# Kernel tuning notes

Hardware: AMD Instinct MI355X
Metric: run time of the kernel (lower is better)

Reference implementation:

```python
import jax, jax.numpy as jnp
import numpy as np

EULER = 0.5772156649015329  # Euler-Mascheroni constant


def _expi_neg(t):
    """Ei(t) for t < 0, via Ei(t) = -E1(-t).

    E1 uses the power series for x < 8 and the asymptotic expansion for x >= 8.
    This replaces the scipy.special.expi CPU round-trip of the original module.
    """
    x = -t  # x > 0
    # --- series branch (x < 8): E1(x) = -gamma - ln(x) + sum_{k>=1} (-1)^{k+1} x^k/(k*k!)
    xs = jnp.minimum(x, 8.0)
    s = jnp.zeros_like(xs)
    term = xs  # (-1)^{k+1} xs^k / k!  starting at k=1
    for k in range(1, 31):
        s = s + term / k
        term = term * (-xs) / (k + 1)
    e1_small = -EULER - jnp.log(xs) + s
    # --- asymptotic branch (x >= 8): E1(x) ~ e^{-x}/x * sum_n (-1)^n n! / x^n
    xl = jnp.maximum(x, 8.0)
    a = jnp.ones_like(xl)
    acc = jnp.ones_like(xl)
    for n in range(1, 9):
        a = a * (-n) / xl
        acc = acc + a
    e1_large = jnp.exp(-xl) / xl * acc
    e1 = jnp.where(x < 8.0, e1_small, e1_large)
    return -e1


def _li(v):
    # logarithmic integral li(v) = Ei(ln v); constant w.r.t. params (scipy detaches in torch)
    return jax.lax.stop_gradient(_expi_neg(jnp.log(v)))


def _phi(u, var2, var3, var4, var5):
    log_term = jnp.log(1.0 - u)
    li_term = _li(1.0 - u)
    return (var2 / log_term
            + var3 * li_term
            + var4 * ((1.0 - u) / log_term - li_term)
            + var5 * ((1.0 - u) * (log_term + 1.0) / (2.0 * log_term ** 2) - li_term / 2.0))


def setup_inputs() -> dict:
    key = jax.random.key(0)
    B, L, D = 262144, 64, 32
    hidden = [128, 128, 64]
    ks = jax.random.split(key, 16)
    u = jax.random.uniform(ks[0], (B, L), dtype=jnp.float32, minval=1e-4, maxval=1.0 - 1e-4)
    dims = [L] + hidden + [D]
    inp = {"u": u}
    for i in range(4):
        inp[f"W{i}"] = jax.random.normal(ks[1 + 2 * i], (dims[i], dims[i + 1]), dtype=jnp.float32) / np.sqrt(dims[i]).astype(np.float32)
        inp[f"b{i}"] = jnp.zeros((dims[i + 1],), dtype=jnp.float32)
    for j in range(1, 7):
        inp[f"var{j}"] = jax.random.normal(ks[8 + j], (1, D), dtype=jnp.float32) * 0.1
    return inp


def reference(u, W0, b0, W1, b1, W2, b2, W3, b3, var1, var2, var3, var4, var5, var6):
    # MLP: three Linear+ReLU blocks then final Linear to dim_data
    h = u
    for W, b in ((W0, b0), (W1, b1), (W2, b2)):
        h = jax.nn.relu(h @ W + b)
    net = h @ W3 + b3  # (B, dim_data)
    D = net.shape[1]
    ud = u[:, :D]
    # spline corrections
    p01 = -4.0 * ud ** 5 + 5.0 * ud ** 4
    corr1 = jnp.nan_to_num(p01 * (var1 + _phi(ud, var2, var3, var4, var5)), nan=0.0)
    corr2 = var6 * (ud ** 3 - 2.0 * ud ** 2 + ud)
    net_tif = jax.nn.relu(net + corr1 + corr2)
    # inverse TIF activation: ((1 - u^2)/2)^{-x}
    return jnp.power((1.0 - ud ** 2) / 2.0, -net_tif)
```

## Files before the change

kernel.cpp:

```cpp
#include <hip/hip_runtime.h>
#include <hip/hip_bf16.h>
#include <math.h>

#define FLT_MAX_F 3.4028234663852886e38f
#define PITCH_H 136

typedef _Float16 half8 __attribute__((ext_vector_type(8)));
typedef __attribute__((ext_vector_type(4))) float f32x4;
typedef __attribute__((ext_vector_type(8))) short short8;

__global__ void prep_weights(const float* __restrict__ W0, const float* __restrict__ W1,
                             const float* __restrict__ W2, const float* __restrict__ W3,
                             short* __restrict__ ws) {
    int e = blockIdx.x * 256 + threadIdx.x;
    const float* W; int N, NT, base, ul;
    if (e < 1024)      { W = W0; N = 128; NT = 8; base = 0;     ul = e; }
    else if (e < 3072) { W = W1; N = 128; NT = 8; base = 8192;  ul = e - 1024; }
    else if (e < 4096) { W = W2; N = 64;  NT = 4; base = 24576; ul = e - 3072; }
    else if (e < 4352) { W = W3; N = 32;  NT = 2; base = 32768; ul = e - 4096; }
    else return;
    const int cp = ul >> 6, lane = ul & 63;
    const int s = cp / NT, ct = cp % NT;
    const int k0 = s * 32 + (lane >> 4) * 8;
    const int n = ct * 16 + (lane & 15);
    union { half8 h; short8 s; } v;
#pragma unroll
    for (int j = 0; j < 8; ++j) v.h[j] = (_Float16)W[(size_t)(k0 + j) * N + n];
    *(short8*)(ws + base + cp * 512 + lane * 8) = v.s;
}

template <int K, int N, int G>
__device__ __forceinline__ void layer_frag(const half8* __restrict__ wf,
                                           const float* __restrict__ bias,
                                           const half8 af[K / 32], int lane, int m,
                                           f32x4* acc) {
    constexpr int NK = K / 32, NT = N / 16, CP = NK * NT, NG = CP / G;
    static_assert(CP % G == 0, "group must divide chunk count");
    half8 buf[2][G];
#pragma unroll
    for (int i = 0; i < G; ++i) buf[0][i] = wf[i * 64 + lane];
#pragma unroll
    for (int ct = 0; ct < NT; ++ct) {
        float b = bias[ct * 16 + m];
        acc[ct] = f32x4{b, b, b, b};
    }
#pragma unroll
    for (int g = 0; g < NG; ++g) {
        constexpr int dummy = 0; (void)dummy;
        const int cur = g & 1, nxt = cur ^ 1;
        if (g + 1 < NG) {
#pragma unroll
            for (int i = 0; i < G; ++i)
                buf[nxt][i] = wf[(size_t)((g + 1) * G + i) * 64 + lane];
        }
#pragma unroll
        for (int i = 0; i < G; ++i) {
            const int cp = g * G + i, s = cp / NT, ct = cp % NT;
            acc[ct] = __builtin_amdgcn_mfma_f32_16x16x32_f16(af[s], buf[cur][i], acc[ct], 0, 0, 0);
        }
    }
}

template <int K>
__device__ __forceinline__ void load_a_lds(const _Float16* __restrict__ lw, int m, int q,
                                           half8 af[K / 32]) {
    const _Float16* rp = lw + m * PITCH_H + q * 8;
#pragma unroll
    for (int s = 0; s < K / 32; ++s) af[s] = *(const half8*)(rp + s * 32);
}

template <int N>
__device__ __forceinline__ void store_d_lds(_Float16* __restrict__ lw, int m, int q,
                                            const f32x4* acc, bool relu) {
#pragma unroll
    for (int ct = 0; ct < N / 16; ++ct) {
#pragma unroll
        for (int r = 0; r < 4; ++r) {
            float v = acc[ct][r];
            if (relu) v = fmaxf(v, 0.0f);
            lw[(q * 4 + r) * PITCH_H + ct * 16 + m] = (_Float16)v;
        }
    }
}

__device__ __forceinline__ float expi_neg_fast(float t) {
    float x = -t;
    float e1s = -__logf(x) + (-0.57721566f + x * (0.99999193f + x * (-0.24991055f
              + x * (0.05519968f + x * (-0.00976004f + x * 0.00107857f)))));
    float num = 0.2677737343f + x * (8.6347608925f + x * (18.0590169730f
              + x * (8.5733287401f + x)));
    float den = 3.9584969228f + x * (21.0996530827f + x * (25.6329561486f
              + x * (9.5733223454f + x)));
    float e1l = __expf(-x) * num * __builtin_amdgcn_rcpf(x * den);
    float e1 = (x < 1.0f) ? e1s : e1l;
    return -e1;
}

__global__ __launch_bounds__(256, 4) void mlp_phi_mfma(
    const float* __restrict__ u,
    const float* __restrict__ b0, const float* __restrict__ b1,
    const float* __restrict__ b2, const float* __restrict__ b3,
    const short* __restrict__ ws,
    const float* __restrict__ var1, const float* __restrict__ var2,
    const float* __restrict__ var3, const float* __restrict__ var4,
    const float* __restrict__ var5, const float* __restrict__ var6,
    float* __restrict__ out) {
    __shared__ __align__(16) _Float16 lds[4 * 16 * PITCH_H];
    const int t = threadIdx.x, lane = t & 63, wave = t >> 6;
    const int m = lane & 15, q = lane >> 4;
    _Float16* lw = lds + wave * 16 * PITCH_H;
    const size_t row0 = (size_t)blockIdx.x * 64 + wave * 16;

    const half8* wf0 = (const half8*)(ws);
    const half8* wf1 = (const half8*)(ws + 8192);
    const half8* wf2 = (const half8*)(ws + 24576);
    const half8* wf3 = (const half8*)(ws + 32768);

    half8 af[4];
    f32x4 acc[8];

    {
        const float* up = u + (row0 + m) * 64;
#pragma unroll
        for (int s = 0; s < 2; ++s) {
            float4 v0 = *(const float4*)(up + s * 32 + q * 8);
            float4 v1 = *(const float4*)(up + s * 32 + q * 8 + 4);
            half8 a;
            a[0] = (_Float16)v0.x; a[1] = (_Float16)v0.y;
            a[2] = (_Float16)v0.z; a[3] = (_Float16)v0.w;
            a[4] = (_Float16)v1.x; a[5] = (_Float16)v1.y;
            a[6] = (_Float16)v1.z; a[7] = (_Float16)v1.w;
            af[s] = a;
        }
    }
    layer_frag<64, 128, 8>(wf0, b0, af, lane, m, acc);
    store_d_lds<128>(lw, m, q, acc, true);

    load_a_lds<128>(lw, m, q, af);
    layer_frag<128, 128, 8>(wf1, b1, af, lane, m, acc);
    store_d_lds<128>(lw, m, q, acc, true);

    load_a_lds<128>(lw, m, q, af);
    layer_frag<128, 64, 8>(wf2, b2, af, lane, m, acc);
    store_d_lds<64>(lw, m, q, acc, true);

    load_a_lds<64>(lw, m, q, af);

    float ue[8];
#pragma unroll
    for (int ot = 0; ot < 2; ++ot)
#pragma unroll
        for (int r = 0; r < 4; ++r)
            ue[ot * 4 + r] = u[(row0 + q * 4 + r) * 64 + ot * 16 + m];

    layer_frag<64, 32, 4>(wf3, b3, af, lane, m, acc);

#pragma unroll
    for (int ot = 0; ot < 2; ++ot) {
        const int d = ot * 16 + m;
        const float v1 = var1[d], v2 = var2[d], v3 = var3[d],
                    v4 = var4[d], v5 = var5[d], v6 = var6[d];
#pragma unroll
        for (int r = 0; r < 4; ++r) {
            const size_t row = row0 + q * 4 + r;
            const float net = acc[ot][r];
            const float ud = ue[ot * 4 + r];

            const float lt = __logf(1.0f - ud);
            const float li = expi_neg_fast(lt);
            const float omu = 1.0f - ud;

            const float rl = __builtin_amdgcn_rcpf(lt);
            const float phi = v2 * rl
                            + v3 * li
                            + v4 * (omu * rl - li)
                            + v5 * (omu * (lt + 1.0f) * 0.5f * (rl * rl) - 0.5f * li);

            const float ud2 = ud * ud;
            const float ud4 = ud2 * ud2;
            const float p01 = -4.0f * ud4 * ud + 5.0f * ud4;

            float corr1 = p01 * (v1 + phi);
            if (isnan(corr1)) {
                corr1 = 0.0f;
            } else if (isinf(corr1)) {
                corr1 = copysignf(FLT_MAX_F, corr1);
            }
            const float corr2 = v6 * (ud * ud2 - 2.0f * ud2 + ud);

            float nt = net + corr1 + corr2;
            nt = fmaxf(nt, 0.0f);

            const float base = (1.0f - ud2) * 0.5f;
            out[row * 32 + d] = __expf(-nt * __logf(base));
        }
    }
}

extern "C" void kernel_launch(void* const* d_in, const int* in_sizes, int n_in,
                              void* d_out, int out_size, void* d_ws, size_t ws_size,
                              hipStream_t stream) {
    const float* u    = (const float*)d_in[0];
    const float* W0   = (const float*)d_in[1];
    const float* b0   = (const float*)d_in[2];
    const float* W1   = (const float*)d_in[3];
    const float* b1   = (const float*)d_in[4];
    const float* W2   = (const float*)d_in[5];
    const float* b2   = (const float*)d_in[6];
    const float* W3   = (const float*)d_in[7];
    const float* b3   = (const float*)d_in[8];
    const float* var1 = (const float*)d_in[9];
    const float* var2 = (const float*)d_in[10];
    const float* var3 = (const float*)d_in[11];
    const float* var4 = (const float*)d_in[12];
    const float* var5 = (const float*)d_in[13];
    const float* var6 = (const float*)d_in[14];
    float* out = (float*)d_out;
    short* ws = (short*)d_ws;

    prep_weights<<<dim3(17), dim3(256), 0, stream>>>(W0, W1, W2, W3, ws);

    const int B = in_sizes[0] / 64;
    const int blocks = B / 64;
    mlp_phi_mfma<<<dim3(blocks), dim3(256), 0, stream>>>(
        u, b0, b1, b2, b3, ws,
        var1, var2, var3, var4, var5, var6, out);
}
```

Before: 168.8 us.

## Process two 16-row tiles per wave to reuse weight fragments across MFMAs

Each wave now handles 32 rows (two M-tiles), so every weight fragment loaded from global memory feeds two MFMA instructions, halving weight traffic per row. The explicit double-buffered prefetch is replaced by direct per-chunk loads, and occupancy bounds drop to 2 blocks per CU with twice the LDS per block. The epilogue is also simplified algebraically (merged li coefficients, log2/exp2 intrinsics, removed nan/inf clamping). Dropping the nan/inf handling could change outputs for edge inputs, and register pressure roughly doubles.

```diff
diff --git a/kernel.cpp b/kernel.cpp
--- a/kernel.cpp
+++ b/kernel.cpp
@@ -2,8 +2,8 @@
 #include <hip/hip_bf16.h>
 #include <math.h>
 
-#define FLT_MAX_F 3.4028234663852886e38f
 #define PITCH_H 136
+#define LN2_F 0.69314718055994531f
 
 typedef _Float16 half8 __attribute__((ext_vector_type(8)));
 typedef __attribute__((ext_vector_type(4))) float f32x4;
@@ -29,41 +29,32 @@
     *(short8*)(ws + base + cp * 512 + lane * 8) = v.s;
 }
 
-template <int K, int N, int G>
-__device__ __forceinline__ void layer_frag(const half8* __restrict__ wf,
-                                           const float* __restrict__ bias,
-                                           const half8 af[K / 32], int lane, int m,
-                                           f32x4* acc) {
-    constexpr int NK = K / 32, NT = N / 16, CP = NK * NT, NG = CP / G;
-    static_assert(CP % G == 0, "group must divide chunk count");
-    half8 buf[2][G];
-#pragma unroll
-    for (int i = 0; i < G; ++i) buf[0][i] = wf[i * 64 + lane];
+template <int K, int N>
+__device__ __forceinline__ void layer_frag2(const half8* __restrict__ wf,
+                                            const float* __restrict__ bias,
+                                            const half8 (&af)[2][4], int lane, int m,
+                                            f32x4 (&acc)[2][8]) {
+    constexpr int NK = K / 32, NT = N / 16;
 #pragma unroll
     for (int ct = 0; ct < NT; ++ct) {
         float b = bias[ct * 16 + m];
-        acc[ct] = f32x4{b, b, b, b};
-    }
-#pragma unroll
-    for (int g = 0; g < NG; ++g) {
-        constexpr int dummy = 0; (void)dummy;
-        const int cur = g & 1, nxt = cur ^ 1;
-        if (g + 1 < NG) {
-#pragma unroll
-            for (int i = 0; i < G; ++i)
-                buf[nxt][i] = wf[(size_t)((g + 1) * G + i) * 64 + lane];
-        }
-#pragma unroll
-        for (int i = 0; i < G; ++i) {
-            const int cp = g * G + i, s = cp / NT, ct = cp % NT;
-            acc[ct] = __builtin_amdgcn_mfma_f32_16x16x32_f16(af[s], buf[cur][i], acc[ct], 0, 0, 0);
+        acc[0][ct] = f32x4{b, b, b, b};
+        acc[1][ct] = f32x4{b, b, b, b};
+    }
+#pragma unroll
+    for (int s = 0; s < NK; ++s) {
+#pragma unroll
+        for (int ct = 0; ct < NT; ++ct) {
+            half8 bh = wf[(size_t)(s * NT + ct) * 64 + lane];
+            acc[0][ct] = __builtin_amdgcn_mfma_f32_16x16x32_f16(af[0][s], bh, acc[0][ct], 0, 0, 0);
+            acc[1][ct] = __builtin_amdgcn_mfma_f32_16x16x32_f16(af[1][s], bh, acc[1][ct], 0, 0, 0);
         }
     }
 }
 
 template <int K>
 __device__ __forceinline__ void load_a_lds(const _Float16* __restrict__ lw, int m, int q,
-                                           half8 af[K / 32]) {
+                                           half8 af[4]) {
     const _Float16* rp = lw + m * PITCH_H + q * 8;
 #pragma unroll
     for (int s = 0; s < K / 32; ++s) af[s] = *(const half8*)(rp + s * 32);
@@ -83,20 +74,7 @@
     }
 }
 
-__device__ __forceinline__ float expi_neg_fast(float t) {
-    float x = -t;
-    float e1s = -__logf(x) + (-0.57721566f + x * (0.99999193f + x * (-0.24991055f
-              + x * (0.05519968f + x * (-0.00976004f + x * 0.00107857f)))));
-    float num = 0.2677737343f + x * (8.6347608925f + x * (18.0590169730f
-              + x * (8.5733287401f + x)));
-    float den = 3.9584969228f + x * (21.0996530827f + x * (25.6329561486f
-              + x * (9.5733223454f + x)));
-    float e1l = __expf(-x) * num * __builtin_amdgcn_rcpf(x * den);
-    float e1 = (x < 1.0f) ? e1s : e1l;
-    return -e1;
-}
-
-__global__ __launch_bounds__(256, 4) void mlp_phi_mfma(
+__global__ __launch_bounds__(256, 2) void mlp_phi_mfma(
     const float* __restrict__ u,
     const float* __restrict__ b0, const float* __restrict__ b1,
     const float* __restrict__ b2, const float* __restrict__ b3,
@@ -105,22 +83,23 @@
     const float* __restrict__ var3, const float* __restrict__ var4,
     const float* __restrict__ var5, const float* __restrict__ var6,
     float* __restrict__ out) {
-    __shared__ __align__(16) _Float16 lds[4 * 16 * PITCH_H];
+    __shared__ __align__(16) _Float16 lds[4 * 32 * PITCH_H];
     const int t = threadIdx.x, lane = t & 63, wave = t >> 6;
     const int m = lane & 15, q = lane >> 4;
-    _Float16* lw = lds + wave * 16 * PITCH_H;
-    const size_t row0 = (size_t)blockIdx.x * 64 + wave * 16;
+    _Float16* lw = lds + wave * 32 * PITCH_H;
+    const size_t row0 = (size_t)blockIdx.x * 128 + wave * 32;
 
     const half8* wf0 = (const half8*)(ws);
     const half8* wf1 = (const half8*)(ws + 8192);
     const half8* wf2 = (const half8*)(ws + 24576);
     const half8* wf3 = (const half8*)(ws + 32768);
 
-    half8 af[4];
-    f32x4 acc[8];
-
-    {
-        const float* up = u + (row0 + m) * 64;
+    half8 af[2][4];
+    f32x4 acc[2][8];
+
+#pragma unroll
+    for (int mt = 0; mt < 2; ++mt) {
+        const float* up = u + (row0 + mt * 16 + m) * 64;
 #pragma unroll
         for (int s = 0; s < 2; ++s) {
             float4 v0 = *(const float4*)(up + s * 32 + q * 8);
@@ -130,69 +109,84 @@
             a[2] = (_Float16)v0.z; a[3] = (_Float16)v0.w;
             a[4] = (_Float16)v1.x; a[5] = (_Float16)v1.y;
             a[6] = (_Float16)v1.z; a[7] = (_Float16)v1.w;
-            af[s] = a;
-        }
-    }
-    layer_frag<64, 128, 8>(wf0, b0, af, lane, m, acc);
-    store_d_lds<128>(lw, m, q, acc, true);
-
-    load_a_lds<128>(lw, m, q, af);
-    layer_frag<128, 128, 8>(wf1, b1, af, lane, m, acc);
-    store_d_lds<128>(lw, m, q, acc, true);
-
-    load_a_lds<128>(lw, m, q, af);
-    layer_frag<128, 64, 8>(wf2, b2, af, lane, m, acc);
-    store_d_lds<64>(lw, m, q, acc, true);
-
-    load_a_lds<64>(lw, m, q, af);
-
-    float ue[8];
-#pragma unroll
-    for (int ot = 0; ot < 2; ++ot)
-#pragma unroll
-        for (int r = 0; r < 4; ++r)
-            ue[ot * 4 + r] = u[(row0 + q * 4 + r) * 64 + ot * 16 + m];
-
-    layer_frag<64, 32, 4>(wf3, b3, af, lane, m, acc);
+            af[mt][s] = a;
+        }
+    }
+    layer_frag2<64, 128>(wf0, b0, af, lane, m, acc);
+#pragma unroll
+    for (int mt = 0; mt < 2; ++mt) store_d_lds<128>(lw + mt * 16 * PITCH_H, m, q, acc[mt], true);
+
+#pragma unroll
+    for (int mt = 0; mt < 2; ++mt) load_a_lds<128>(lw + mt * 16 * PITCH_H, m, q, af[mt]);
+    layer_frag2<128, 128>(wf1, b1, af, lane, m, acc);
+#pragma unroll
+    for (int mt = 0; mt < 2; ++mt) store_d_lds<128>(lw + mt * 16 * PITCH_H, m, q, acc[mt], true);
+
+#pragma unroll
+    for (int mt = 0; mt < 2; ++mt) load_a_lds<128>(lw + mt * 16 * PITCH_H, m, q, af[mt]);
+    layer_frag2<128, 64>(wf2, b2, af, lane, m, acc);
+#pragma unroll
+    for (int mt = 0; mt < 2; ++mt) store_d_lds<64>(lw + mt * 16 * PITCH_H, m, q, acc[mt], true);
+
+#pragma unroll
+    for (int mt = 0; mt < 2; ++mt) load_a_lds<64>(lw + mt * 16 * PITCH_H, m, q, af[mt]);
+
+    float ue[2][8];
+#pragma unroll
+    for (int mt = 0; mt < 2; ++mt)
+#pragma unroll
+        for (int ot = 0; ot < 2; ++ot)
+#pragma unroll
+            for (int r = 0; r < 4; ++r)
+                ue[mt][ot * 4 + r] = u[(row0 + mt * 16 + q * 4 + r) * 64 + ot * 16 + m];
+
+    layer_frag2<64, 32>(wf3, b3, af, lane, m, acc);
 
 #pragma unroll
     for (int ot = 0; ot < 2; ++ot) {
         const int d = ot * 16 + m;
         const float v1 = var1[d], v2 = var2[d], v3 = var3[d],
-                    v4 = var4[d], v5 = var5[d], v6 = var6[d];
-#pragma unroll
-        for (int r = 0; r < 4; ++r) {
-            const size_t row = row0 + q * 4 + r;
-            const float net = acc[ot][r];
-            const float ud = ue[ot * 4 + r];
-
-            const float lt = __logf(1.0f - ud);
-            const float li = expi_neg_fast(lt);
-            const float omu = 1.0f - ud;
-
-            const float rl = __builtin_amdgcn_rcpf(lt);
-            const float phi = v2 * rl
-                            + v3 * li
-                            + v4 * (omu * rl - li)
-                            + v5 * (omu * (lt + 1.0f) * 0.5f * (rl * rl) - 0.5f * li);
-
-            const float ud2 = ud * ud;
-            const float ud4 = ud2 * ud2;
-            const float p01 = -4.0f * ud4 * ud + 5.0f * ud4;
-
-            float corr1 = p01 * (v1 + phi);
-            if (isnan(corr1)) {
-                corr1 = 0.0f;
-            } else if (isinf(corr1)) {
-                corr1 = copysignf(FLT_MAX_F, corr1);
+                    v4 = var4[d], v6 = var6[d];
+        const float v5h = 0.5f * var5[d];
+        const float c3 = v3 - v4 - v5h;
+#pragma unroll
+        for (int mt = 0; mt < 2; ++mt) {
+#pragma unroll
+            for (int r = 0; r < 4; ++r) {
+                const size_t row = row0 + mt * 16 + q * 4 + r;
+                const float net = acc[mt][ot][r];
+                const float ud = ue[mt][ot * 4 + r];
+
+                const float omu = 1.0f - ud;
+                const float lt = __log2f(omu) * LN2_F;
+                const float x = -lt;
+
+                const float e1s = -__log2f(x) * LN2_F
+                    + (-0.57721566f + x * (0.99999193f + x * (-0.24991055f
+                    + x * (0.05519968f + x * (-0.00976004f + x * 0.00107857f)))));
+                const float num = 0.2677737343f + x * (8.6347608925f + x * (18.0590169730f
+                    + x * (8.5733287401f + x)));
+                const float den = 3.9584969228f + x * (21.0996530827f + x * (25.6329561486f
+                    + x * (9.5733223454f + x)));
+                const float e1l = __expf(-x) * num * __builtin_amdgcn_rcpf(x * den);
+                const float li = -((x < 1.0f) ? e1s : e1l);
+
+                const float rl = __builtin_amdgcn_rcpf(lt);
+                const float phi = fmaf(v4, omu, v2) * rl
+                                + (v5h * omu * (lt + 1.0f)) * rl * rl
+                                + c3 * li;
+
+                const float ud2 = ud * ud;
+                const float ud4 = ud2 * ud2;
+                const float p01 = ud4 * fmaf(-4.0f, ud, 5.0f);
+                const float corr1 = p01 * (v1 + phi);
+                const float d1 = ud - 1.0f;
+                const float corr2 = v6 * ud * d1 * d1;
+
+                const float nt = fmaxf(net + corr1 + corr2, 0.0f);
+                const float base = fmaf(-0.5f, ud2, 0.5f);
+                out[row * 32 + d] = __builtin_amdgcn_exp2f(-nt * __log2f(base));
             }
-            const float corr2 = v6 * (ud * ud2 - 2.0f * ud2 + ud);
-
-            float nt = net + corr1 + corr2;
-            nt = fmaxf(nt, 0.0f);
-
-            const float base = (1.0f - ud2) * 0.5f;
-            out[row * 32 + d] = __expf(-nt * __logf(base));
         }
     }
 }
@@ -221,7 +215,7 @@
     prep_weights<<<dim3(17), dim3(256), 0, stream>>>(W0, W1, W2, W3, ws);
 
     const int B = in_sizes[0] / 64;
-    const int blocks = B / 64;
+    const int blocks = B / 128;
     mlp_phi_mfma<<<dim3(blocks), dim3(256), 0, stream>>>(
         u, b0, b1, b2, b3, ws,
         var1, var2, var3, var4, var5, var6, out);
```

Measured after the change: 160.0 us. 5.2% less time.
